# Kernel tuning notes

Measured on AMD Instinct MI355X. Metric: run time of the kernel, lower is better.

Reference implementation:

```python
import jax, jax.numpy as jnp
import numpy as np

D_MODEL = 1024
IDX_DIM = 64
SEQ = 4096
D_STATE = 64
EXPAND = 1
HEADDIM = 32
D_CONV = 4
D_INNER = EXPAND * D_MODEL
NHEADS = D_INNER // HEADDIM
CONV_DIM = D_INNER + 2 * D_STATE
D_IN_PROJ = 2 * D_INNER + 2 * D_STATE + NHEADS  # z, xBC, dt


def setup_inputs() -> dict:
    key = jax.random.key(0)
    ks = jax.random.split(key, 8)
    def rn(k, shape, scale=1.0):
        return jax.random.normal(k, shape, jnp.float32) * scale
    return {
        "x": rn(ks[0], (SEQ, D_MODEL)),
        "W_in": rn(ks[1], (D_IN_PROJ, D_MODEL), D_MODEL ** -0.5),
        "conv_w": rn(ks[2], (CONV_DIM, D_CONV), D_CONV ** -0.5),
        "conv_b": jnp.zeros((CONV_DIM,), jnp.float32),
        "dt_bias": rn(ks[3], (NHEADS,)),
        "A_log": jnp.log(jnp.arange(1, NHEADS + 1, dtype=jnp.float32)),
        "D": jnp.ones((NHEADS,), jnp.float32),
        "norm_w": jnp.ones((D_INNER,), jnp.float32),
        "W_out": rn(ks[4], (D_MODEL, D_INNER), D_INNER ** -0.5),
        "W_q": rn(ks[5], (IDX_DIM, D_MODEL), D_MODEL ** -0.5),
        "W_k": rn(ks[6], (IDX_DIM, D_MODEL), D_MODEL ** -0.5),
    }


def _silu(v):
    return v * jax.nn.sigmoid(v)


def _mamba2(x, W_in, conv_w, conv_b, dt_bias, A_log, Dp, norm_w, W_out):
    L = x.shape[0]
    zxbcdt = x @ W_in.T  # [L, D_IN_PROJ]
    z, xBC, dt = jnp.split(zxbcdt, [D_INNER, D_INNER + CONV_DIM], axis=-1)
    # depthwise causal conv1d, kernel D_CONV
    xc = jax.lax.conv_general_dilated(
        xBC.T[None],               # [1, C, L]
        conv_w[:, None, :],        # [C, 1, K]
        (1,), [(D_CONV - 1, 0)], feature_group_count=CONV_DIM)[0].T
    xBC = _silu(xc + conv_b)
    xs, B, C = jnp.split(xBC, [D_INNER, D_INNER + D_STATE], axis=-1)
    xs = xs.reshape(L, NHEADS, HEADDIM)
    dt = jax.nn.softplus(dt + dt_bias)   # [L, H]
    A = -jnp.exp(A_log)                  # [H]

    def step(h, inp):
        x_t, B_t, C_t, dt_t = inp        # [H,P], [N], [N], [H]
        dA = jnp.exp(dt_t * A)           # [H]
        h = h * dA[:, None, None] + (dt_t[:, None] * x_t)[:, :, None] * B_t[None, None, :]
        return h, jnp.einsum('hpn,n->hp', h, C_t)

    h0 = jnp.zeros((NHEADS, HEADDIM, D_STATE), x.dtype)
    _, ys = jax.lax.scan(step, h0, (xs, B, C, dt))  # ys: [L, H, P]
    y = ys + Dp[None, :, None] * xs
    y = y.reshape(L, D_INNER)
    y = y * _silu(z)                                 # gated RMSNorm
    y = y * jax.lax.rsqrt(jnp.mean(y * y, axis=-1, keepdims=True) + 1e-5) * norm_w
    return y @ W_out.T


def reference(x, W_in, conv_w, conv_b, dt_bias, A_log, D, norm_w, W_out, W_q, W_k):
    L = x.shape[0]
    x_mamba = _mamba2(x, W_in, conv_w, conv_b, dt_bias, A_log, D, norm_w, W_out)
    q = x_mamba @ W_q.T                  # [L, IDX_DIM]
    k = x @ W_k.T                        # [L, IDX_DIM]
    scores = jnp.einsum('ti,si->ts', q, k) * (IDX_DIM ** -0.5)
    mask = jnp.tril(jnp.ones((L, L), dtype=bool))
    return jnp.where(mask, scores, -jnp.inf)
```

## Files before the change

kernel.cpp:

```cpp
#include <hip/hip_runtime.h>
#include <math.h>

#define L_SEQ 4096
#define DMODEL 1024
#define DINNER 1024
#define DSTATE 64
#define NH 32
#define HD 32
#define CONVD 1152
#define DPROJ2 2272
#define KOFF 2208
#define QC 128
#define NC 32

#define NEG_FILL (-1e30f)

typedef __attribute__((ext_vector_type(8))) short short8;
typedef __attribute__((ext_vector_type(4))) float f32x4;
typedef unsigned short u16;

__device__ __forceinline__ u16 f2bf(float f) {
  unsigned int u = __float_as_uint(f);
  unsigned int r = (u + 0x7fffu + ((u >> 16) & 1u)) >> 16;
  return (u16)r;
}
__device__ __forceinline__ float bf2f(u16 b) {
  unsigned int u = ((unsigned int)b) << 16;
  return __uint_as_float(u);
}
__device__ __forceinline__ short8 pack8(float4 a, float4 b) {
  short8 v;
  v[0] = (short)f2bf(a.x); v[1] = (short)f2bf(a.y);
  v[2] = (short)f2bf(a.z); v[3] = (short)f2bf(a.w);
  v[4] = (short)f2bf(b.x); v[5] = (short)f2bf(b.y);
  v[6] = (short)f2bf(b.z); v[7] = (short)f2bf(b.w);
  return v;
}

__device__ __forceinline__ void g2l16(const void* g, void* l) {
  __builtin_amdgcn_global_load_lds(
      (const __attribute__((address_space(1))) unsigned int*)g,
      (__attribute__((address_space(3))) unsigned int*)l, 16, 0, 0);
}

#define CAST_N0 (L_SEQ * DMODEL / 8)
#define CAST_N1 (2208 * DMODEL / 8)
#define CAST_N2 (64 * DMODEL / 8)
#define CAST_TOTAL (CAST_N0 + CAST_N1 + 2 * CAST_N2)
#define CAST_BLKS (CAST_TOTAL / 256)
__global__ __launch_bounds__(256) void cast_tr_k(const float* __restrict__ x,
                                                 const float* __restrict__ W_in,
                                                 const float* __restrict__ W_k,
                                                 const float* __restrict__ W_q,
                                                 const float* __restrict__ W_out,
                                                 u16* __restrict__ x_bf,
                                                 u16* __restrict__ Wcat,
                                                 u16* __restrict__ Wq_bf,
                                                 u16* __restrict__ WoutT) {
  __shared__ float tile[64][65];
  int bid = blockIdx.x;
  if (bid < CAST_BLKS) {
    int gid = bid * 256 + threadIdx.x;
    const float* src;
    u16* dst;
    int i;
    if (gid < CAST_N0) { src = x; dst = x_bf; i = gid; }
    else if (gid < CAST_N0 + CAST_N1) { src = W_in; dst = Wcat; i = gid - CAST_N0; }
    else if (gid < CAST_N0 + CAST_N1 + CAST_N2) {
      src = W_k; dst = Wcat + (size_t)2208 * DMODEL; i = gid - CAST_N0 - CAST_N1;
    } else { src = W_q; dst = Wq_bf; i = gid - CAST_N0 - CAST_N1 - CAST_N2; }
    i *= 8;
    float4 f0 = *(const float4*)(src + i);
    float4 f1 = *(const float4*)(src + i + 4);
    *(short8*)(dst + i) = pack8(f0, f1);
    return;
  }
  bid -= CAST_BLKS;
  int bx = bid & 15, by = bid >> 4;
  int tx = threadIdx.x & 63, ty = threadIdx.x >> 6;
#pragma unroll
  for (int k = 0; k < 16; k++) {
    int r = ty + k * 4;
    tile[r][tx] = W_out[(size_t)(by * 64 + r) * 1024 + bx * 64 + tx];
  }
  __syncthreads();
#pragma unroll
  for (int k = 0; k < 16; k++) {
    int r = ty + k * 4;
    WoutT[(size_t)(bx * 64 + r) * 1024 + by * 64 + tx] = f2bf(tile[tx][r]);
  }
}

#define GEMM_BLKS 576
__global__ __launch_bounds__(256) void gemm_wqo_k(const u16* __restrict__ A,
                                                  const u16* __restrict__ B,
                                                  u16* __restrict__ Cbf,
                                                  const u16* __restrict__ Wq,
                                                  const u16* __restrict__ WoutT,
                                                  const float* __restrict__ nw,
                                                  u16* __restrict__ Wqo) {
  __shared__ u16 As[128 * 64];
  __shared__ u16 Bs[128 * 64];
  const int tid = threadIdx.x;
  const int wave = tid >> 6, lane = tid & 63;
  const int l15 = lane & 15, quad = lane >> 4;
  const int wg = blockIdx.x;
  if (wg >= GEMM_BLKS) {
    const int j0 = (wg - GEMM_BLKS) * 64;
    f32x4 acc[4] = {};
    for (int kk = 0; kk < 32; kk++) {
      short8 b = *(const short8*)(WoutT + (size_t)(j0 + wave * 16 + l15) * 1024 + kk * 32 + quad * 8);
#pragma unroll
      for (int mi = 0; mi < 4; mi++) {
        short8 a = *(const short8*)(Wq + (size_t)(mi * 16 + l15) * 1024 + kk * 32 + quad * 8);
        acc[mi] = __builtin_amdgcn_mfma_f32_16x16x32_bf16(a, b, acc[mi], 0, 0, 0);
      }
    }
    int col = j0 + wave * 16 + l15;
    float w = nw[col];
#pragma unroll
    for (int mi = 0; mi < 4; mi++)
#pragma unroll
      for (int r = 0; r < 4; r++) {
        int i = mi * 16 + quad * 4 + r;
        Wqo[(size_t)i * 1024 + col] = f2bf(acc[mi][r] * w);
      }
    return;
  }
  const int N = DPROJ2, K = DMODEL;
  const int m0 = (wg & 31) * 128, n0 = (wg >> 5) * 128;
  const int wm = (wave >> 1) * 64, wn = (wave & 1) * 64;

  const u16* aptr[4];
  const u16* bptr[4];
  char *ldsA[4], *ldsB[4];
#pragma unroll
  for (int b = 0; b < 4; b++) {
    int ch = b * 256 + tid;
    int row = ch >> 3, q = (ch & 7) ^ (row & 7);
    aptr[b] = A + (size_t)(m0 + row) * K + q * 8;
    int bn = min(n0 + row, N - 1);
    bptr[b] = B + (size_t)bn * K + q * 8;
    ldsA[b] = (char*)As + b * 4096 + wave * 1024;
    ldsB[b] = (char*)Bs + b * 4096 + wave * 1024;
  }

  int offA[2][4], offB[2][4];
#pragma unroll
  for (int kk = 0; kk < 2; kk++)
#pragma unroll
    for (int i = 0; i < 4; i++) {
      int ra = wm + i * 16 + l15;
      offA[kk][i] = ra * 64 + ((kk * 4 + quad) ^ (ra & 7)) * 8;
      int rb = wn + i * 16 + l15;
      offB[kk][i] = rb * 64 + ((kk * 4 + quad) ^ (rb & 7)) * 8;
    }

  f32x4 acc[4][4] = {};
  for (int k0 = 0; k0 < K; k0 += 64) {
#pragma unroll
    for (int b = 0; b < 4; b++) g2l16(aptr[b] + k0, ldsA[b]);
#pragma unroll
    for (int b = 0; b < 4; b++) g2l16(bptr[b] + k0, ldsB[b]);
    __builtin_amdgcn_s_waitcnt(0);
    __syncthreads();
#pragma unroll
    for (int kk = 0; kk < 2; kk++) {
      short8 af[4], bfr[4];
#pragma unroll
      for (int i = 0; i < 4; i++) af[i] = *(const short8*)(As + offA[kk][i]);
#pragma unroll
      for (int j = 0; j < 4; j++) bfr[j] = *(const short8*)(Bs + offB[kk][j]);
#pragma unroll
      for (int mi = 0; mi < 4; mi++)
#pragma unroll
        for (int ni = 0; ni < 4; ni++)
          acc[mi][ni] = __builtin_amdgcn_mfma_f32_16x16x32_bf16(af[mi], bfr[ni],
                                                                acc[mi][ni], 0, 0, 0);
    }
    __syncthreads();
  }
#pragma unroll
  for (int mi = 0; mi < 4; mi++)
#pragma unroll
    for (int r = 0; r < 4; r++) {
      int grow = m0 + wm + mi * 16 + quad * 4 + r;
#pragma unroll
      for (int ni = 0; ni < 4; ni++) {
        int gcol = n0 + wn + ni * 16 + l15;
        if (gcol < N) Cbf[(size_t)grow * N + gcol] = f2bf(acc[mi][ni][r]);
      }
    }
}

__global__ __launch_bounds__(256) void splitk64(const u16* __restrict__ A,
                                                const u16* __restrict__ B,
                                                float* __restrict__ P,
                                                int M, int K) {
  __shared__ u16 As[128 * 32];
  __shared__ u16 Bs[64 * 32];
  const int tid = threadIdx.x;
  const int wave = tid >> 6, lane = tid & 63;
  const int m0 = blockIdx.x * 128;
  const int ks = blockIdx.y;
  const int wm = (wave >> 1) * 64, wn = (wave & 1) * 32;
  const int l15 = lane & 15, quad = lane >> 4;

  const int c0 = tid, c1 = 256 + tid;
  const int r0 = c0 >> 2, q0 = (c0 & 3) ^ ((r0 >> 1) & 3);
  const int r1 = c1 >> 2, q1 = (c1 & 3) ^ ((r1 >> 1) & 3);
  const int rb = tid >> 2, qb = (tid & 3) ^ ((rb >> 1) & 3);
  const u16* a0 = A + (size_t)(m0 + r0) * K + q0 * 8;
  const u16* a1 = A + (size_t)(m0 + r1) * K + q1 * 8;
  const u16* bptr = B + (size_t)rb * K + qb * 8;
  char* ldsA0 = (char*)As + wave * 1024;
  char* ldsA1 = (char*)As + 4096 + wave * 1024;
  char* ldsB = (char*)Bs + wave * 1024;

  int offA[4], offB[2];
#pragma unroll
  for (int i = 0; i < 4; i++) {
    int ra = wm + i * 16 + l15;
    offA[i] = ra * 32 + (quad ^ ((ra >> 1) & 3)) * 8;
  }
#pragma unroll
  for (int j = 0; j < 2; j++) {
    int rr = wn + j * 16 + l15;
    offB[j] = rr * 32 + (quad ^ ((rr >> 1) & 3)) * 8;
  }

  f32x4 acc[4][2] = {};
  const int kbeg = ks * 128;
  for (int k0 = kbeg; k0 < kbeg + 128; k0 += 32) {
    g2l16(a0 + k0, ldsA0);
    g2l16(a1 + k0, ldsA1);
    g2l16(bptr + k0, ldsB);
    __builtin_amdgcn_s_waitcnt(0);
    __syncthreads();
    short8 af[4], bfr[2];
#pragma unroll
    for (int i = 0; i < 4; i++) af[i] = *(const short8*)(As + offA[i]);
#pragma unroll
    for (int j = 0; j < 2; j++) bfr[j] = *(const short8*)(Bs + offB[j]);
#pragma unroll
    for (int mi = 0; mi < 4; mi++)
#pragma unroll
      for (int ni = 0; ni < 2; ni++)
        acc[mi][ni] = __builtin_amdgcn_mfma_f32_16x16x32_bf16(af[mi], bfr[ni],
                                                              acc[mi][ni], 0, 0, 0);
    __syncthreads();
  }
  float* Pp = P + (size_t)ks * M * 64;
#pragma unroll
  for (int mi = 0; mi < 4; mi++)
#pragma unroll
    for (int r = 0; r < 4; r++) {
      int grow = m0 + wm + mi * 16 + quad * 4 + r;
#pragma unroll
      for (int ni = 0; ni < 2; ni++)
        Pp[(size_t)grow * 64 + wn + ni * 16 + l15] = acc[mi][ni][r];
    }
}

__global__ __launch_bounds__(256) void reduce8_k(const float* __restrict__ P,
                                                 const float* __restrict__ ssq,
                                                 u16* __restrict__ out, int n) {
  int i = blockIdx.x * 256 + threadIdx.x;
  if (i >= n) return;
  float s = 0.f;
#pragma unroll
  for (int ks = 0; ks < 8; ks++) s += P[(size_t)ks * n + i];
  float sc = rsqrtf(ssq[i >> 6] * (1.f / 1024.f) + 1e-5f) * 0.125f;
  out[i] = f2bf(s * sc);
}

#define CONVB 2304
#define KDB 128
__global__ __launch_bounds__(256) void conv_dt_k(const u16* __restrict__ zx,
                                                 const float* __restrict__ cw,
                                                 const float* __restrict__ cb,
                                                 u16* __restrict__ xbc,
                                                 u16* __restrict__ kd,
                                                 const float* __restrict__ dt_bias,
                                                 const float* __restrict__ A_log,
                                                 float* __restrict__ dtsp,
                                                 float* __restrict__ aL,
                                                 float* __restrict__ ssq) {
  int bid = blockIdx.x, tid = threadIdx.x;
  if (bid < CONVB) {
    int tblk = bid / 9, cgb = bid - tblk * 9;
    int t = tblk * 16 + (tid >> 4);
    int c0 = (cgb * 16 + (tid & 15)) * 8;
    float acc[8];
#pragma unroll
    for (int j = 0; j < 8; j++) acc[j] = cb[c0 + j];
    float wv[8][4];
#pragma unroll
    for (int j = 0; j < 8; j++) {
      float4 w4 = *(const float4*)(cw + (c0 + j) * 4);
      wv[j][0] = w4.x; wv[j][1] = w4.y; wv[j][2] = w4.z; wv[j][3] = w4.w;
    }
#pragma unroll
    for (int k = 0; k < 4; k++) {
      int s = t - 3 + k;
      if (s >= 0) {
        short8 v = *(const short8*)(zx + (size_t)s * DPROJ2 + DINNER + c0);
#pragma unroll
        for (int j = 0; j < 8; j++) acc[j] += bf2f((u16)v[j]) * wv[j][k];
      }
    }
    short8 o;
#pragma unroll
    for (int j = 0; j < 8; j++) o[j] = (short)f2bf(acc[j] / (1.f + expf(-acc[j])));
    *(short8*)(xbc + (size_t)t * CONVD + c0) = o;
    return;
  }
  if (bid < CONVB + KDB) {
    int gid = (bid - CONVB) * 256 + tid;
    int t = gid >> 3, c0 = (gid & 7) * 8;
    *(short8*)(kd + (size_t)t * 64 + c0) =
        *(const short8*)(zx + (size_t)t * DPROJ2 + KOFF + c0);
    return;
  }
  int dblk = bid - CONVB - KDB;
  if (tid < 16) ssq[dblk * 16 + tid] = 0.f;
  int w = tid >> 6, lane = tid & 63;
  int idx = dblk * 4 + w;
  int h = idx & 31, c = idx >> 5;
  float negA = -expf(A_log[h]);
  float bias = dt_bias[h];
  float carry = 0.f;
#pragma unroll
  for (int seg = 0; seg < 2; seg++) {
    int t = c * QC + seg * 64 + lane;
    float xv = bf2f(zx[(size_t)t * DPROJ2 + 2176 + h]) + bias;
    float sp = (xv > 20.f) ? xv : log1pf(expf(xv));
    dtsp[(size_t)t * 32 + h] = sp;
    float v = sp * negA;
#pragma unroll
    for (int off = 1; off < 64; off <<= 1) {
      float u = __shfl_up(v, off, 64);
      if (lane >= off) v += u;
    }
    aL[(size_t)t * 32 + h] = carry + v;
    carry += __shfl(v, 63, 64);
  }
}

__global__ __launch_bounds__(256) void csg_k(const u16* __restrict__ xbc,
                                             const float* __restrict__ dtsp,
                                             const float* __restrict__ aL,
                                             u16* __restrict__ S,
                                             u16* __restrict__ G,
                                             float* __restrict__ out) {
  int tid = threadIdx.x;
  const int wave = tid >> 6, lane = tid & 63;
  const int l15 = lane & 15, quad = lane >> 4;
  __shared__ __align__(16) u16 sXs[32 * 136];
  __shared__ __align__(16) u16 sBT[64 * 136];
  __shared__ float scoef[QC];
  if (blockIdx.x < (unsigned)(NC * NH)) {
    int h = blockIdx.x & 31, c = blockIdx.x >> 5;
    if (tid < QC) {
      float aend = aL[(size_t)(c * QC + QC - 1) * 32 + h];
      float a = aL[(size_t)(c * QC + tid) * 32 + h];
      scoef[tid] = expf(aend - a) * dtsp[(size_t)(c * QC + tid) * 32 + h];
    }
    __syncthreads();
    for (int j = tid; j < 32 * QC / 8; j += 256) {
      int s = j & 127, p0 = (j >> 7) * 8;
      short8 v = *(const short8*)(xbc + (size_t)(c * QC + s) * CONVD + h * HD + p0);
      float cf = scoef[s];
#pragma unroll
      for (int e = 0; e < 8; e++) sXs[(p0 + e) * 136 + s] = f2bf(cf * bf2f((u16)v[e]));
    }
    for (int j = tid; j < 64 * QC / 8; j += 256) {
      int s = j & 127, n0 = (j >> 7) * 8;
      short8 v = *(const short8*)(xbc + (size_t)(c * QC + s) * CONVD + DINNER + n0);
#pragma unroll
      for (int e = 0; e < 8; e++) sBT[(n0 + e) * 136 + s] = (u16)v[e];
    }
    __syncthreads();
    f32x4 acc[2] = {};
#pragma unroll
    for (int kk = 0; kk < 4; kk++) {
      short8 b = *(const short8*)(sBT + (wave * 16 + l15) * 136 + kk * 32 + quad * 8);
#pragma unroll
      for (int i = 0; i < 2; i++) {
        short8 a = *(const short8*)(sXs + (i * 16 + l15) * 136 + kk * 32 + quad * 8);
        acc[i] = __builtin_amdgcn_mfma_f32_16x16x32_bf16(a, b, acc[i], 0, 0, 0);
      }
    }
    u16* Sb = S + ((size_t)c * 32 + h) * 2048;
#pragma unroll
    for (int i = 0; i < 2; i++)
#pragma unroll
      for (int r = 0; r < 4; r++) {
        int p = i * 16 + quad * 4 + r;
        Sb[p * 64 + wave * 16 + l15] = f2bf(acc[i][r]);
      }
    return;
  }
  if (blockIdx.x < (unsigned)(NC * NH + NC)) {
    int c = blockIdx.x - NC * NH;
    const int wm = (wave >> 1) * 64, wn = (wave & 1) * 64;
    f32x4 acc[4][4] = {};
#pragma unroll
    for (int kk = 0; kk < 2; kk++) {
      short8 a[4], b[4];
#pragma unroll
      for (int i = 0; i < 4; i++) {
        int t = wm + i * 16 + l15;
        a[i] = *(const short8*)(xbc + (size_t)(c * QC + t) * CONVD + DINNER + DSTATE + kk * 32 + quad * 8);
        int s = wn + i * 16 + l15;
        b[i] = *(const short8*)(xbc + (size_t)(c * QC + s) * CONVD + DINNER + kk * 32 + quad * 8);
      }
#pragma unroll
      for (int mi = 0; mi < 4; mi++)
#pragma unroll
        for (int ni = 0; ni < 4; ni++)
          acc[mi][ni] = __builtin_amdgcn_mfma_f32_16x16x32_bf16(a[mi], b[ni],
                                                                acc[mi][ni], 0, 0, 0);
    }
    u16* Gb = G + (size_t)c * QC * QC;
#pragma unroll
    for (int mi = 0; mi < 4; mi++)
#pragma unroll
      for (int r = 0; r < 4; r++) {
        int t = wm + mi * 16 + quad * 4 + r;
#pragma unroll
        for (int ni = 0; ni < 4; ni++)
          Gb[(size_t)t * QC + wn + ni * 16 + l15] = f2bf(acc[mi][ni][r]);
      }
    return;
  }
  int f = blockIdx.x - (NC * NH + NC);
  int u = f / 31, v = f - u * 31;
  int by, bx;
  if (v >= u) { by = u; bx = v + 1; }
  else { by = 31 - u; bx = 32 - u + v; }
  int m0 = by * 128, n0 = bx * 128;
  f32x4 fl = {NEG_FILL, NEG_FILL, NEG_FILL, NEG_FILL};
  for (int i = tid; i < 128 * 32; i += 256) {
    int row = i >> 5, c4 = (i & 31) << 2;
    __builtin_nontemporal_store(fl, (f32x4*)(out + (size_t)(m0 + row) * L_SEQ + n0 + c4));
  }
}

__global__ __launch_bounds__(256) void state_scan_k(const u16* __restrict__ S,
                                                    const float* __restrict__ aL,
                                                    u16* __restrict__ Hinit) {
  int idx = blockIdx.x * 256 + threadIdx.x;
  int h = idx >> 11, rem = idx & 2047;
  float E = 0.f;
#pragma unroll
  for (int c = 0; c < NC; c++) {
    size_t o = ((size_t)c * 32 + h) * 2048 + rem;
    Hinit[o] = f2bf(E);
    float dec = expf(aL[(size_t)(c * QC + QC - 1) * 32 + h]);
    E = E * dec + bf2f(S[o]);
  }
}

__global__ __launch_bounds__(256) void yout_mfma(const u16* __restrict__ xbc,
                                                 const float* __restrict__ dtsp,
                                                 const float* __restrict__ aL,
                                                 const u16* __restrict__ G,
                                                 const u16* __restrict__ Hinit,
                                                 const float* __restrict__ Dv,
                                                 const u16* __restrict__ zx,
                                                 float* __restrict__ ssq,
                                                 u16* __restrict__ y) {
  int h = blockIdx.x & 31, c = blockIdx.x >> 5;
  int tid = threadIdx.x;
  __shared__ __align__(16) u16 sXT[32 * 136];
  __shared__ float sa[QC];
  __shared__ float sd[QC];

  if (tid < QC) {
    sa[tid] = aL[(size_t)(c * QC + tid) * 32 + h];
    sd[tid] = dtsp[(size_t)(c * QC + tid) * 32 + h];
  }
  for (int j = tid; j < 32 * QC / 8; j += 256) {
    int t = j & 127, p0 = (j >> 7) * 8;
    short8 v = *(const short8*)(xbc + (size_t)(c * QC + t) * CONVD + h * HD + p0);
#pragma unroll
    for (int e = 0; e < 8; e++) sXT[(p0 + e) * 136 + t] = (u16)v[e];
  }
  __syncthreads();

  const int wave = tid >> 6, lane = tid & 63;
  const int l15 = lane & 15, quad = lane >> 4;
  f32x4 acc1[2][2] = {};
  f32x4 acc2[2][2] = {};

#pragma unroll
  for (int kk = 0; kk < 4; kk++) {
    short8 b[2];
#pragma unroll
    for (int j = 0; j < 2; j++)
      b[j] = *(const short8*)(sXT + (j * 16 + l15) * 136 + kk * 32 + quad * 8);
#pragma unroll
    for (int i = 0; i < 2; i++) {
      int rmax = wave * 32 + i * 16 + 15;
      if (kk * 32 > rmax) continue;
      int m = wave * 32 + i * 16 + l15;
      float am = sa[m];
      short8 g8 = *(const short8*)(G + (size_t)c * QC * QC + (size_t)m * QC + kk * 32 + quad * 8);
      int s0 = kk * 32 + quad * 8;
      short8 a;
#pragma unroll
      for (int j2 = 0; j2 < 8; j2++) {
        int s = s0 + j2;
        float w = 0.f;
        if (s <= m) w = expf(am - sa[s]) * sd[s] * bf2f((u16)g8[j2]);
        a[j2] = (short)f2bf(w);
      }
#pragma unroll
      for (int j = 0; j < 2; j++)
        acc1[i][j] = __builtin_amdgcn_mfma_f32_16x16x32_bf16(a, b[j], acc1[i][j], 0, 0, 0);
    }
  }

  const u16* Hbase = Hinit + ((size_t)c * 32 + h) * 2048;
#pragma unroll
  for (int kk = 0; kk < 2; kk++) {
    short8 b[2];
#pragma unroll
    for (int j = 0; j < 2; j++)
      b[j] = *(const short8*)(Hbase + (size_t)(j * 16 + l15) * 64 + kk * 32 + quad * 8);
#pragma unroll
    for (int i = 0; i < 2; i++) {
      int t = wave * 32 + i * 16 + l15;
      short8 a = *(const short8*)(xbc + (size_t)(c * QC + t) * CONVD + DINNER + DSTATE + kk * 32 + quad * 8);
#pragma unroll
      for (int j = 0; j < 2; j++)
        acc2[i][j] = __builtin_amdgcn_mfma_f32_16x16x32_bf16(a, b[j], acc2[i][j], 0, 0, 0);
    }
  }

  float Dh = Dv[h];
#pragma unroll
  for (int i = 0; i < 2; i++) {
#pragma unroll
    for (int r = 0; r < 4; r++) {
      int t = wave * 32 + i * 16 + quad * 4 + r;
      float et = expf(sa[t]);
      float part = 0.f;
#pragma unroll
      for (int j = 0; j < 2; j++) {
        int p = j * 16 + l15;
        float xv = bf2f(sXT[p * 136 + t]);
        float val = acc1[i][j][r] + et * acc2[i][j][r] + Dh * xv;
        float z = bf2f(zx[(size_t)(c * QC + t) * DPROJ2 + h * HD + p]);
        float vg = val * (z / (1.f + expf(-z)));
        part += vg * vg;
        y[(size_t)(c * QC + t) * DINNER + h * HD + p] = f2bf(vg);
      }
      part += __shfl_xor(part, 1, 64);
      part += __shfl_xor(part, 2, 64);
      part += __shfl_xor(part, 4, 64);
      part += __shfl_xor(part, 8, 64);
      if (l15 == 0) atomicAdd(ssq + c * QC + t, part);
    }
  }
}

__global__ __launch_bounds__(256) void scores_mfma(const u16* __restrict__ q,
                                                   const u16* __restrict__ kd,
                                                   float* __restrict__ out) {
  const int m0 = blockIdx.y * 128, n0 = blockIdx.x * 128;
  if (n0 > m0 + 127) return;
  const int tid = threadIdx.x;
  const int wave = tid >> 6, lane = tid & 63;
  const int wm = (wave >> 1) * 64, wn = (wave & 1) * 64;
  const int l15 = lane & 15, quad = lane >> 4;
  f32x4 acc[4][4] = {};
#pragma unroll
  for (int kk = 0; kk < 2; kk++) {
    short8 a[4], b[4];
#pragma unroll
    for (int i = 0; i < 4; i++) {
      a[i] = *(const short8*)(q + (size_t)(m0 + wm + i * 16 + l15) * 64 + kk * 32 + quad * 8);
      b[i] = *(const short8*)(kd + (size_t)(n0 + wn + i * 16 + l15) * 64 + kk * 32 + quad * 8);
    }
#pragma unroll
    for (int mi = 0; mi < 4; mi++)
#pragma unroll
      for (int ni = 0; ni < 4; ni++)
        acc[mi][ni] = __builtin_amdgcn_mfma_f32_16x16x32_bf16(a[mi], b[ni],
                                                              acc[mi][ni], 0, 0, 0);
  }
#pragma unroll
  for (int mi = 0; mi < 4; mi++)
#pragma unroll
    for (int r = 0; r < 4; r++) {
      int row = m0 + wm + mi * 16 + quad * 4 + r;
#pragma unroll
      for (int ni = 0; ni < 4; ni++) {
        int col = n0 + wn + ni * 16 + l15;
        float val = (col <= row) ? acc[mi][ni][r] : NEG_FILL;
        __builtin_nontemporal_store(val, out + (size_t)row * L_SEQ + col);
      }
    }
}

extern "C" void kernel_launch(void* const* d_in, const int* in_sizes, int n_in,
                              void* d_out, int out_size, void* d_ws, size_t ws_size,
                              hipStream_t stream) {
  const float* x       = (const float*)d_in[0];
  const float* W_in    = (const float*)d_in[1];
  const float* conv_w  = (const float*)d_in[2];
  const float* conv_b  = (const float*)d_in[3];
  const float* dt_bias = (const float*)d_in[4];
  const float* A_log   = (const float*)d_in[5];
  const float* Dv      = (const float*)d_in[6];
  const float* norm_w  = (const float*)d_in[7];
  const float* W_out   = (const float*)d_in[8];
  const float* W_q     = (const float*)d_in[9];
  const float* W_k     = (const float*)d_in[10];
  float* out = (float*)d_out;

  char* ws = (char*)d_ws;
  size_t off = 0;
  auto alloc = [&](size_t bytes) {
    void* p = (void*)(ws + off);
    off += (bytes + 255) & ~(size_t)255;
    return p;
  };
  u16* zx_bf    = (u16*)alloc((size_t)L_SEQ * DPROJ2 * 2);
  u16* xbc_bf   = (u16*)alloc((size_t)L_SEQ * CONVD * 2);
  float* dtsp   = (float*)alloc((size_t)L_SEQ * NH * 4);
  float* aL     = (float*)alloc((size_t)L_SEQ * NH * 4);
  u16* S        = (u16*)alloc((size_t)NC * NH * HD * DSTATE * 2);
  u16* Hinit    = (u16*)alloc((size_t)NC * NH * HD * DSTATE * 2);
  u16* G        = (u16*)alloc((size_t)NC * QC * QC * 2);
  float* ssq    = (float*)alloc((size_t)L_SEQ * 4);
  u16* y1_bf    = (u16*)alloc((size_t)L_SEQ * DINNER * 2);
  u16* kd_bf    = (u16*)alloc((size_t)L_SEQ * 64 * 2);
  u16* x_bf     = (u16*)alloc((size_t)L_SEQ * DMODEL * 2);
  u16* Wcat_bf  = (u16*)alloc((size_t)DPROJ2 * DMODEL * 2);
  u16* WoutT_bf = (u16*)alloc((size_t)DMODEL * DINNER * 2);
  u16* Wq_bf    = (u16*)alloc((size_t)64 * DMODEL * 2);
  u16* Wqo_bf   = (u16*)alloc((size_t)64 * DINNER * 2);
  u16* q_bf     = (u16*)alloc((size_t)L_SEQ * 64 * 2);
  float* Pq     = (float*)alloc((size_t)8 * L_SEQ * 64 * 4);

  cast_tr_k<<<dim3(CAST_BLKS + 256), 256, 0, stream>>>(x, W_in, W_k, W_q, W_out,
                                                       x_bf, Wcat_bf, Wq_bf, WoutT_bf);
  gemm_wqo_k<<<dim3(GEMM_BLKS + 16), 256, 0, stream>>>(x_bf, Wcat_bf, zx_bf,
                                                       Wq_bf, WoutT_bf, norm_w, Wqo_bf);
  conv_dt_k<<<dim3(CONVB + KDB + 256), 256, 0, stream>>>(
      zx_bf, conv_w, conv_b, xbc_bf, kd_bf, dt_bias, A_log, dtsp, aL, ssq);
  csg_k<<<dim3(NC * NH + NC + 496), 256, 0, stream>>>(xbc_bf, dtsp, aL, S, G, out);
  state_scan_k<<<dim3(NH * HD * DSTATE / 256), 256, 0, stream>>>(S, aL, Hinit);
  yout_mfma<<<dim3(NC * NH), 256, 0, stream>>>(xbc_bf, dtsp, aL, G, Hinit, Dv,
                                               zx_bf, ssq, y1_bf);
  splitk64<<<dim3(L_SEQ / 128, 8), 256, 0, stream>>>(y1_bf, Wqo_bf, Pq, L_SEQ, DINNER);
  reduce8_k<<<dim3(L_SEQ * 64 / 256), 256, 0, stream>>>(Pq, ssq, q_bf, L_SEQ * 64);
  scores_mfma<<<dim3(32, 32), 256, 0, stream>>>(q_bf, kd_bf, out);
}
```

Baseline: 218.8 us.

## Split yout_mfma chunks into two time halves and precompute gate in shared memory

The yout kernel now launches two blocks per (chunk, head), each covering 64 time rows, so each wave handles one 16-row tile instead of two. The first half loads only the first 64 columns of the transposed x tile, which trims redundant causal work. The SiLU gate of z is computed once with coalesced vector loads into shared memory, and exp(aL) is precomputed per row, replacing the scattered per-element zx loads in the epilogue. The second half still reloads all 128 columns of x, so some loads and setup are duplicated across blocks.

```diff
diff --git a/kernel.cpp b/kernel.cpp
--- a/kernel.cpp
+++ b/kernel.cpp
@@ -471,55 +471,71 @@
                                                  const u16* __restrict__ zx,
                                                  float* __restrict__ ssq,
                                                  u16* __restrict__ y) {
-  int h = blockIdx.x & 31, c = blockIdx.x >> 5;
-  int tid = threadIdx.x;
+  const int bid = blockIdx.x;
+  const int tb = bid & 1, h = (bid >> 1) & 31, c = bid >> 6;
+  const int t0 = tb * 64;
+  const int tid = threadIdx.x;
   __shared__ __align__(16) u16 sXT[32 * 136];
   __shared__ float sa[QC];
   __shared__ float sd[QC];
+  __shared__ float se[64];
+  __shared__ float sgate[64][32];
 
   if (tid < QC) {
     sa[tid] = aL[(size_t)(c * QC + tid) * 32 + h];
     sd[tid] = dtsp[(size_t)(c * QC + tid) * 32 + h];
-  }
-  for (int j = tid; j < 32 * QC / 8; j += 256) {
-    int t = j & 127, p0 = (j >> 7) * 8;
-    short8 v = *(const short8*)(xbc + (size_t)(c * QC + t) * CONVD + h * HD + p0);
-#pragma unroll
-    for (int e = 0; e < 8; e++) sXT[(p0 + e) * 136 + t] = (u16)v[e];
+  } else if (tid < QC + 64) {
+    int t = tid - QC;
+    se[t] = expf(aL[(size_t)(c * QC + t0 + t) * 32 + h]);
+  }
+  {
+    int t = tid >> 2, p0 = (tid & 3) * 8;
+    short8 v = *(const short8*)(zx + (size_t)(c * QC + t0 + t) * DPROJ2 + h * HD + p0);
+#pragma unroll
+    for (int e = 0; e < 8; e++) {
+      float z = bf2f((u16)v[e]);
+      sgate[t][p0 + e] = z / (1.f + expf(-z));
+    }
+  }
+  const int SMAX = t0 + 64;
+  const int lg = 6 + tb;
+  for (int j = tid; j < 32 * SMAX / 8; j += 256) {
+    int s = j & (SMAX - 1), p0 = (j >> lg) * 8;
+    short8 v = *(const short8*)(xbc + (size_t)(c * QC + s) * CONVD + h * HD + p0);
+#pragma unroll
+    for (int e = 0; e < 8; e++) sXT[(p0 + e) * 136 + s] = (u16)v[e];
   }
   __syncthreads();
 
   const int wave = tid >> 6, lane = tid & 63;
   const int l15 = lane & 15, quad = lane >> 4;
-  f32x4 acc1[2][2] = {};
-  f32x4 acc2[2][2] = {};
+  const int trow = t0 + wave * 16;
+  const int rmax = trow + 15;
+  f32x4 acc1[2] = {};
+  f32x4 acc2[2] = {};
 
 #pragma unroll
   for (int kk = 0; kk < 4; kk++) {
+    if (kk * 32 > rmax) continue;
     short8 b[2];
 #pragma unroll
     for (int j = 0; j < 2; j++)
       b[j] = *(const short8*)(sXT + (j * 16 + l15) * 136 + kk * 32 + quad * 8);
-#pragma unroll
-    for (int i = 0; i < 2; i++) {
-      int rmax = wave * 32 + i * 16 + 15;
-      if (kk * 32 > rmax) continue;
-      int m = wave * 32 + i * 16 + l15;
-      float am = sa[m];
-      short8 g8 = *(const short8*)(G + (size_t)c * QC * QC + (size_t)m * QC + kk * 32 + quad * 8);
-      int s0 = kk * 32 + quad * 8;
-      short8 a;
-#pragma unroll
-      for (int j2 = 0; j2 < 8; j2++) {
-        int s = s0 + j2;
-        float w = 0.f;
-        if (s <= m) w = expf(am - sa[s]) * sd[s] * bf2f((u16)g8[j2]);
-        a[j2] = (short)f2bf(w);
-      }
-#pragma unroll
-      for (int j = 0; j < 2; j++)
-        acc1[i][j] = __builtin_amdgcn_mfma_f32_16x16x32_bf16(a, b[j], acc1[i][j], 0, 0, 0);
-    }
+    int m = trow + l15;
+    float am = sa[m];
+    short8 g8 = *(const short8*)(G + (size_t)c * QC * QC + (size_t)m * QC + kk * 32 + quad * 8);
+    int s0 = kk * 32 + quad * 8;
+    short8 a;
+#pragma unroll
+    for (int j2 = 0; j2 < 8; j2++) {
+      int s = s0 + j2;
+      float w = 0.f;
+      if (s <= m) w = expf(am - sa[s]) * sd[s] * bf2f((u16)g8[j2]);
+      a[j2] = (short)f2bf(w);
+    }
+#pragma unroll
+    for (int j = 0; j < 2; j++)
+      acc1[j] = __builtin_amdgcn_mfma_f32_16x16x32_bf16(a, b[j], acc1[j], 0, 0, 0);
   }
 
   const u16* Hbase = Hinit + ((size_t)c * 32 + h) * 2048;
@@ -529,40 +545,33 @@
 #pragma unroll
     for (int j = 0; j < 2; j++)
       b[j] = *(const short8*)(Hbase + (size_t)(j * 16 + l15) * 64 + kk * 32 + quad * 8);
-#pragma unroll
-    for (int i = 0; i < 2; i++) {
-      int t = wave * 32 + i * 16 + l15;
-      short8 a = *(const short8*)(xbc + (size_t)(c * QC + t) * CONVD + DINNER + DSTATE + kk * 32 + quad * 8);
-#pragma unroll
-      for (int j = 0; j < 2; j++)
-        acc2[i][j] = __builtin_amdgcn_mfma_f32_16x16x32_bf16(a, b[j], acc2[i][j], 0, 0, 0);
-    }
+    int t = trow + l15;
+    short8 a = *(const short8*)(xbc + (size_t)(c * QC + t) * CONVD + DINNER + DSTATE + kk * 32 + quad * 8);
+#pragma unroll
+    for (int j = 0; j < 2; j++)
+      acc2[j] = __builtin_amdgcn_mfma_f32_16x16x32_bf16(a, b[j], acc2[j], 0, 0, 0);
   }
 
   float Dh = Dv[h];
 #pragma unroll
-  for (int i = 0; i < 2; i++) {
-#pragma unroll
-    for (int r = 0; r < 4; r++) {
-      int t = wave * 32 + i * 16 + quad * 4 + r;
-      float et = expf(sa[t]);
-      float part = 0.f;
-#pragma unroll
-      for (int j = 0; j < 2; j++) {
-        int p = j * 16 + l15;
-        float xv = bf2f(sXT[p * 136 + t]);
-        float val = acc1[i][j][r] + et * acc2[i][j][r] + Dh * xv;
-        float z = bf2f(zx[(size_t)(c * QC + t) * DPROJ2 + h * HD + p]);
-        float vg = val * (z / (1.f + expf(-z)));
-        part += vg * vg;
-        y[(size_t)(c * QC + t) * DINNER + h * HD + p] = f2bf(vg);
-      }
-      part += __shfl_xor(part, 1, 64);
-      part += __shfl_xor(part, 2, 64);
-      part += __shfl_xor(part, 4, 64);
-      part += __shfl_xor(part, 8, 64);
-      if (l15 == 0) atomicAdd(ssq + c * QC + t, part);
-    }
+  for (int r = 0; r < 4; r++) {
+    int tt = trow + quad * 4 + r;
+    float et = se[tt - t0];
+    float part = 0.f;
+#pragma unroll
+    for (int j = 0; j < 2; j++) {
+      int p = j * 16 + l15;
+      float xv = bf2f(sXT[p * 136 + tt]);
+      float val = acc1[j][r] + et * acc2[j][r] + Dh * xv;
+      float vg = val * sgate[tt - t0][p];
+      part += vg * vg;
+      y[(size_t)(c * QC + tt) * DINNER + h * HD + p] = f2bf(vg);
+    }
+    part += __shfl_xor(part, 1, 64);
+    part += __shfl_xor(part, 2, 64);
+    part += __shfl_xor(part, 4, 64);
+    part += __shfl_xor(part, 8, 64);
+    if (l15 == 0) atomicAdd(ssq + c * QC + tt, part);
   }
 }
 
@@ -654,8 +663,8 @@
       zx_bf, conv_w, conv_b, xbc_bf, kd_bf, dt_bias, A_log, dtsp, aL, ssq);
   csg_k<<<dim3(NC * NH + NC + 496), 256, 0, stream>>>(xbc_bf, dtsp, aL, S, G, out);
   state_scan_k<<<dim3(NH * HD * DSTATE / 256), 256, 0, stream>>>(S, aL, Hinit);
-  yout_mfma<<<dim3(NC * NH), 256, 0, stream>>>(xbc_bf, dtsp, aL, G, Hinit, Dv,
-                                               zx_bf, ssq, y1_bf);
+  yout_mfma<<<dim3(NC * NH * 2), 256, 0, stream>>>(xbc_bf, dtsp, aL, G, Hinit, Dv,
+                                                   zx_bf, ssq, y1_bf);
   splitk64<<<dim3(L_SEQ / 128, 8), 256, 0, stream>>>(y1_bf, Wqo_bf, Pq, L_SEQ, DINNER);
   reduce8_k<<<dim3(L_SEQ * 64 / 256), 256, 0, stream>>>(Pq, ssq, q_bf, L_SEQ * 64);
   scores_mfma<<<dim3(32, 32), 256, 0, stream>>>(q_bf, kd_bf, out);
```

Result: slower. 223.5 us (+2.2%).
